# Optimization experiments

Hardware: AMD Instinct MI355X
Metric: run time of the kernel (lower is better)

Reference implementation:

```python
import jax, jax.numpy as jnp
import numpy as np

N = 100000
E = 1600000
IN_DIM, HID, OUT, HEADS, EDGE_DIM = 64, 32, 32, 4, 1


def setup_inputs() -> dict:
    key = jax.random.key(0)
    ks = jax.random.split(key, 24)
    p = lambda k, shape: (jax.random.normal(k, shape, dtype=jnp.float32) * 0.1)
    inp = {
        "x": jax.random.normal(ks[0], (N, IN_DIM), dtype=jnp.float32),
        "edge_index": jax.random.randint(ks[1], (2, E), 0, N, dtype=jnp.int32),
        "edge_attr": jax.random.uniform(ks[2], (E, EDGE_DIM), dtype=jnp.float32),
        # BatchNorm1d(edge_dim), eval mode
        "bn_gamma": jnp.ones((EDGE_DIM,), jnp.float32),
        "bn_beta": jnp.zeros((EDGE_DIM,), jnp.float32),
        "bn_mean": jnp.zeros((EDGE_DIM,), jnp.float32),
        "bn_var": jnp.ones((EDGE_DIM,), jnp.float32),
        # GATConv layer 1: in_dim -> hidden, heads=4, concat
        "W1": p(ks[3], (IN_DIM, HEADS * HID)),
        "as1": p(ks[4], (HEADS, HID)),
        "ad1": p(ks[5], (HEADS, HID)),
        "We1": p(ks[6], (EDGE_DIM, HEADS * HID)),
        "ae1": p(ks[7], (HEADS, HID)),
        "b1": jnp.zeros((HEADS * HID,), jnp.float32),
        # GATConv layer 2: heads*hidden -> out, heads=1, no concat
        "W2": p(ks[8], (HEADS * HID, OUT)),
        "as2": p(ks[9], (1, OUT)),
        "ad2": p(ks[10], (1, OUT)),
        "We2": p(ks[11], (EDGE_DIM, OUT)),
        "ae2": p(ks[12], (1, OUT)),
        "b2": jnp.zeros((OUT,), jnp.float32),
        # feature decoder MLP
        "Wd1": p(ks[13], (OUT, HID)),
        "bd1": jnp.zeros((HID,), jnp.float32),
        "Wd2": p(ks[14], (HID, IN_DIM)),
        "bd2": jnp.zeros((IN_DIM,), jnp.float32),
    }
    return inp


def gat_layer(x, src, dst, e, W, a_src, a_dst, We, a_e, b, heads, out_ch, concat):
    n = x.shape[0]
    h = (x @ W).reshape(n, heads, out_ch)                     # [N,H,C]
    alpha_src = (h * a_src).sum(-1)                           # [N,H]
    alpha_dst = (h * a_dst).sum(-1)                           # [N,H]
    he = (e @ We).reshape(-1, heads, out_ch)                  # [E,H,C]
    alpha = alpha_src[src] + alpha_dst[dst] + (he * a_e).sum(-1)  # [E,H]
    alpha = jax.nn.leaky_relu(alpha, 0.2)
    # segment softmax over destination node
    amax = jax.ops.segment_max(alpha, dst, num_segments=n)
    amax = jnp.where(jnp.isfinite(amax), amax, 0.0)
    ex = jnp.exp(alpha - amax[dst])
    denom = jax.ops.segment_sum(ex, dst, num_segments=n)
    att = ex / (denom[dst] + 1e-16)                           # [E,H]
    msg = h[src] * att[:, :, None]                            # [E,H,C]
    out = jax.ops.segment_sum(msg, dst, num_segments=n)       # [N,H,C]
    out = out.reshape(n, heads * out_ch) if concat else out.mean(axis=1)
    return out + b


def reference(x, edge_index, edge_attr, bn_gamma, bn_beta, bn_mean, bn_var,
              W1, as1, ad1, We1, ae1, b1, W2, as2, ad2, We2, ae2, b2,
              Wd1, bd1, Wd2, bd2):
    src, dst = edge_index[0], edge_index[1]
    # edge_norm(log1p(edge_attr)) with BatchNorm1d in eval mode
    e = (jnp.log1p(edge_attr) - bn_mean) * jax.lax.rsqrt(bn_var + 1e-5) * bn_gamma + bn_beta
    # encoder (dropout inactive in eval)
    h = gat_layer(x, src, dst, e, W1, as1, ad1, We1, ae1, b1, HEADS, HID, True)
    h = jax.nn.elu(h)
    z = gat_layer(h, src, dst, e, W2, as2, ad2, We2, ae2, b2, 1, OUT, False)
    # feature decoder MLP
    x_hat = jax.nn.elu(z @ Wd1 + bd1) @ Wd2 + bd2
    return (z, x_hat)
```

## Files before the change

kernel.cpp:

```cpp
#include <hip/hip_runtime.h>
#include <hip/hip_fp16.h>
#include <math.h>

#define NN 100000
#define NE 1600000

__global__ void k_hist(const int* __restrict__ ei, int* __restrict__ counts,
                       int* __restrict__ rank) {
    int e = blockIdx.x * blockDim.x + threadIdx.x;
    if (e < NE) rank[e] = atomicAdd(&counts[ei[NE + e]], 1);
}

__global__ void k_s1(const int* __restrict__ counts, int* __restrict__ bsum) {
    __shared__ int sd[256];
    int tid = threadIdx.x, b = blockIdx.x;
    int base = b * 2048 + tid * 8;
    int s = 0;
    #pragma unroll
    for (int j = 0; j < 8; ++j) {
        int g = base + j;
        s += (g < NN) ? counts[g] : 0;
    }
    sd[tid] = s;
    __syncthreads();
    for (int d = 128; d; d >>= 1) {
        if (tid < d) sd[tid] += sd[tid + d];
        __syncthreads();
    }
    if (tid == 0) bsum[b] = sd[0];
}

__global__ void k_s2(const int* __restrict__ bsum, int* __restrict__ boff,
                     int* __restrict__ rowptr,
                     const float* __restrict__ We1, const float* __restrict__ ae1,
                     const float* __restrict__ We2, const float* __restrict__ ae2,
                     float* __restrict__ wdot) {
    int t = threadIdx.x;
    if (t == 0) {
        int run = 0;
        for (int b = 0; b < 49; ++b) { boff[b] = run; run += bsum[b]; }
        rowptr[NN] = NE;
    }
    if (t >= 64 && t < 68) {
        int h = t - 64;
        float s = 0.f;
        for (int c = 0; c < 32; ++c) s += We1[h*32+c] * ae1[h*32+c];
        wdot[h] = s;
    } else if (t == 68) {
        float s = 0.f;
        for (int c = 0; c < 32; ++c) s += We2[c] * ae2[c];
        wdot[4] = s;
    }
}

__global__ void k_s3(const int* __restrict__ counts, const int* __restrict__ boff,
                     int* __restrict__ rowptr) {
    __shared__ int sT[256];
    int tid = threadIdx.x, b = blockIdx.x;
    int base = b * 2048 + tid * 8;
    int c[8];
    int s = 0;
    #pragma unroll
    for (int j = 0; j < 8; ++j) {
        int g = base + j;
        c[j] = (g < NN) ? counts[g] : 0;
        s += c[j];
    }
    sT[tid] = s;
    __syncthreads();
    for (int d = 1; d < 256; d <<= 1) {
        int v = (tid >= d) ? sT[tid - d] : 0;
        __syncthreads();
        sT[tid] += v;
        __syncthreads();
    }
    int run = (tid ? sT[tid - 1] : 0) + boff[b];
    #pragma unroll
    for (int j = 0; j < 8; ++j) {
        int g = base + j;
        if (g < NN) rowptr[g] = run;
        run += c[j];
    }
}

__global__ void k_scatter(const int* __restrict__ ei, const float* __restrict__ ea,
                          const float* __restrict__ g, const float* __restrict__ b,
                          const float* __restrict__ m, const float* __restrict__ v,
                          const int* __restrict__ rowptr, const int* __restrict__ rank,
                          int2* __restrict__ edges) {
    int e = blockIdx.x * blockDim.x + threadIdx.x;
    if (e >= NE) return;
    int dst = ei[NE + e];
    int pos = rowptr[dst] + rank[e];
    float en = (log1pf(ea[e]) - m[0]) * rsqrtf(v[0] + 1e-5f) * g[0] + b[0];
    edges[pos] = make_int2(ei[e], __float_as_int(en));
}

__global__ void __launch_bounds__(256, 2)
k1_node1(const float* __restrict__ x, const float* __restrict__ W1,
         const float* __restrict__ as1, const float* __restrict__ ad1,
         __half2* __restrict__ h1h, float* __restrict__ as1n,
         float* __restrict__ ad1n) {
    int tid = threadIdx.x, wid = tid >> 6, lane = tid & 63;
    float wc0[64], wc1[64];
    #pragma unroll
    for (int k = 0; k < 64; ++k) {
        wc0[k] = W1[k*128 + 2*lane];
        wc1[k] = W1[k*128 + 2*lane + 1];
    }
    float asc0 = as1[2*lane], asc1 = as1[2*lane+1];
    float adc0 = ad1[2*lane], adc1 = ad1[2*lane+1];
    int gw = (blockIdx.x << 2) + wid;
    int nw = gridDim.x << 2;
    for (int n = gw; n < NN; n += nw) {
        int nu = __builtin_amdgcn_readfirstlane(n);
        const float* xr = x + (size_t)nu * 64;
        float a0 = 0.f, a1 = 0.f;
        #pragma unroll
        for (int k = 0; k < 64; ++k) {
            float xk = xr[k];
            a0 = fmaf(xk, wc0[k], a0);
            a1 = fmaf(xk, wc1[k], a1);
        }
        h1h[(size_t)nu*64 + lane] = __float22half2_rn(make_float2(a0, a1));
        float p = a0*asc0 + a1*asc1;
        float q = a0*adc0 + a1*adc1;
        #pragma unroll
        for (int d = 1; d < 16; d <<= 1) {
            p += __shfl_xor(p, d);
            q += __shfl_xor(q, d);
        }
        if ((lane & 15) == 0) {
            int h = lane >> 4;
            as1n[nu*4 + h] = p;
            ad1n[nu*4 + h] = q;
        }
    }
}

__global__ void __launch_bounds__(256)
kA1(const int* __restrict__ rowptr, const int2* __restrict__ edges,
    const float* __restrict__ as1n, const float* __restrict__ ad1n,
    const float* __restrict__ wdot, const __half2* __restrict__ h1h,
    const float* __restrict__ b1, const float* __restrict__ W2,
    const float* __restrict__ as2, const float* __restrict__ ad2,
    __half2* __restrict__ h2h, float* __restrict__ as2n, float* __restrict__ ad2n) {
    __shared__ __half2 W2h[64*32];
    __shared__ float4 exs4[4][64];
    __shared__ int    srcl[4][64];
    __shared__ float  slot[4][128];
    int tid = threadIdx.x, wid = tid >> 6, lane = tid & 63;
    for (int i = tid; i < 2048; i += 256) {
        int k2 = i >> 5, c = i & 31;
        W2h[i] = __floats2half2_rn(W2[(2*k2)*32 + c], W2[(2*k2+1)*32 + c]);
    }
    __syncthreads();

    int n = blockIdx.x * 4 + wid;
    int row0 = rowptr[n], row1 = rowptr[n + 1];
    float4 wd  = *(const float4*)wdot;
    float4 adv = *(const float4*)&ad1n[n*4];
    int es = lane >> 5;
    int cq = lane & 31;
    int hq = cq >> 3;
    float den0 = 0.f, den1 = 0.f, den2 = 0.f, den3 = 0.f;
    float4 acc = make_float4(0.f, 0.f, 0.f, 0.f);
    const float* exf = (const float*)&exs4[wid][0];
    const uint2* h1u = (const uint2*)h1h;

    for (int base = row0; base < row1; base += 64) {
        int j = base + lane;
        bool val = j < row1;
        int2 ep = val ? edges[j] : make_int2(0, 0);
        int sv = ep.x;
        float ev = __int_as_float(ep.y);
        float4 asv = *(const float4*)&as1n[sv*4];
        float a0 = asv.x + adv.x + ev*wd.x; a0 = fmaxf(a0, 0.2f*a0);
        float a1 = asv.y + adv.y + ev*wd.y; a1 = fmaxf(a1, 0.2f*a1);
        float a2 = asv.z + adv.z + ev*wd.z; a2 = fmaxf(a2, 0.2f*a2);
        float a3 = asv.w + adv.w + ev*wd.w; a3 = fmaxf(a3, 0.2f*a3);
        float p0 = val ? __expf(a0) : 0.f; den0 += p0;
        float p1 = val ? __expf(a1) : 0.f; den1 += p1;
        float p2 = val ? __expf(a2) : 0.f; den2 += p2;
        float p3 = val ? __expf(a3) : 0.f; den3 += p3;
        exs4[wid][lane] = make_float4(p0, p1, p2, p3);
        srcl[wid][lane] = sv;

        int cnt = min(64, row1 - base);
        for (int i = 0; i < cnt; i += 2) {
            int idx = i + es;
            bool ok = idx < cnt;
            int s = srcl[wid][ok ? idx : i];
            float ex = ok ? exf[idx*4 + hq] : 0.f;
            uint2 u = h1u[(size_t)s*32 + cq];
            float2 hv01 = __half22float2(*(const __half2*)&u.x);
            float2 hv23 = __half22float2(*(const __half2*)&u.y);
            acc.x = fmaf(ex, hv01.x, acc.x);
            acc.y = fmaf(ex, hv01.y, acc.y);
            acc.z = fmaf(ex, hv23.x, acc.z);
            acc.w = fmaf(ex, hv23.y, acc.w);
        }
    }
    acc.x += __shfl_xor(acc.x, 32); acc.y += __shfl_xor(acc.y, 32);
    acc.z += __shfl_xor(acc.z, 32); acc.w += __shfl_xor(acc.w, 32);
    #pragma unroll
    for (int d = 32; d; d >>= 1) {
        den0 += __shfl_xor(den0, d); den1 += __shfl_xor(den1, d);
        den2 += __shfl_xor(den2, d); den3 += __shfl_xor(den3, d);
    }
    float dh = (hq == 0) ? den0 : (hq == 1) ? den1 : (hq == 2) ? den2 : den3;
    float r = 1.f / (dh + 1e-16f);
    float4 b1v = ((const float4*)b1)[cq];
    float o0 = acc.x * r + b1v.x; o0 = o0 > 0.f ? o0 : expm1f(o0);
    float o1 = acc.y * r + b1v.y; o1 = o1 > 0.f ? o1 : expm1f(o1);
    float o2 = acc.z * r + b1v.z; o2 = o2 > 0.f ? o2 : expm1f(o2);
    float o3 = acc.w * r + b1v.w; o3 = o3 > 0.f ? o3 : expm1f(o3);
    if (es == 0) *(float4*)&slot[wid][4*cq] = make_float4(o0, o1, o2, o3);

    int k2base = es * 32;
    float s2 = 0.f;
    #pragma unroll
    for (int kk = 0; kk < 32; ++kk) {
        float2 wf = __half22float2(W2h[(k2base + kk)*32 + cq]);
        s2 = fmaf(slot[wid][2*(k2base + kk)],     wf.x, s2);
        s2 = fmaf(slot[wid][2*(k2base + kk) + 1], wf.y, s2);
    }
    s2 += __shfl_xor(s2, 32);
    int l4 = lane & 15;
    float za = __shfl(s2, 2*l4);
    float zb = __shfl(s2, 2*l4 + 1);
    if (lane < 16) h2h[(size_t)n*16 + l4] = __float22half2_rn(make_float2(za, zb));
    float av = s2 * as2[cq] * 0.5f;
    float dv = s2 * ad2[cq] * 0.5f;
    #pragma unroll
    for (int d = 32; d; d >>= 1) { av += __shfl_xor(av, d); dv += __shfl_xor(dv, d); }
    if (lane == 0) { as2n[n] = av; ad2n[n] = dv; }
}

__global__ void __launch_bounds__(256)
kA2(const int* __restrict__ rowptr, const int2* __restrict__ edges,
    const float* __restrict__ as2n, const float* __restrict__ ad2n,
    const float* __restrict__ wdot, const __half2* __restrict__ h2h,
    const float* __restrict__ b2, const float* __restrict__ Wd1,
    const float* __restrict__ bd1, const float* __restrict__ Wd2,
    const float* __restrict__ bd2, float* __restrict__ out) {
    __shared__ float Wd1s[32*32], Wd2s[32*64];
    __shared__ float pl[4][64];
    __shared__ int   srcl[4][64];
    __shared__ float zs[4][32], ts[4][32];
    int tid = threadIdx.x, wid = tid >> 6, lane = tid & 63;
    int g = lane >> 4, l4 = lane & 15;
    int half = lane >> 5, l5 = lane & 31;
    for (int i = tid; i < 1024; i += 256) Wd1s[i] = Wd1[i];
    for (int i = tid; i < 2048; i += 256) Wd2s[i] = Wd2[i];
    __syncthreads();

    int n = blockIdx.x * 4 + wid;
    int row0 = rowptr[n], row1 = rowptr[n + 1];
    float wd4 = wdot[4];
    float adn = ad2n[n];
    float den = 0.f, acc0 = 0.f, acc1 = 0.f;

    for (int base = row0; base < row1; base += 64) {
        int j = base + lane;
        bool val = j < row1;
        int2 ep = val ? edges[j] : make_int2(0, 0);
        int sv = ep.x;
        float ev = __int_as_float(ep.y);
        float a = as2n[sv] + adn + ev * wd4;
        a = fmaxf(a, 0.2f*a);
        float p = val ? __expf(a) : 0.f;
        den += p;
        pl[wid][lane] = p;
        srcl[wid][lane] = sv;

        int cnt = min(64, row1 - base);
        for (int i = 0; i < cnt; i += 4) {
            int idx = i + g;
            bool ok = idx < cnt;
            int se   = ok ? srcl[wid][idx] : 0;
            float ex = ok ? pl[wid][idx] : 0.f;
            __half2 hv = h2h[(size_t)se*16 + l4];
            float2 hf = __half22float2(hv);
            acc0 = fmaf(ex, hf.x, acc0);
            acc1 = fmaf(ex, hf.y, acc1);
        }
    }
    #pragma unroll
    for (int d = 32; d; d >>= 1) den += __shfl_xor(den, d);
    acc0 += __shfl_xor(acc0, 16); acc0 += __shfl_xor(acc0, 32);
    acc1 += __shfl_xor(acc1, 16); acc1 += __shfl_xor(acc1, 32);
    float r = 1.f / (den + 1e-16f);
    if (lane < 16) {
        float z0 = acc0 * r + b2[2*l4];
        float z1 = acc1 * r + b2[2*l4 + 1];
        *(float2*)&out[(size_t)n*32 + 2*l4] = make_float2(z0, z1);
        *(float2*)&zs[wid][2*l4] = make_float2(z0, z1);
    }
    int kk0 = half * 16;
    float t2 = 0.f;
    #pragma unroll
    for (int k = 0; k < 16; ++k)
        t2 = fmaf(zs[wid][kk0 + k], Wd1s[(kk0 + k)*32 + l5], t2);
    t2 += __shfl_xor(t2, 32);
    t2 += bd1[l5];
    t2 = t2 > 0.f ? t2 : expm1f(t2);
    if (lane < 32) ts[wid][l5] = t2;

    float xo = bd2[lane];
    #pragma unroll
    for (int k = 0; k < 32; ++k)
        xo = fmaf(ts[wid][k], Wd2s[k*64 + lane], xo);
    out[(size_t)NN*32 + (size_t)n*64 + lane] = xo;
}

extern "C" void kernel_launch(void* const* d_in, const int* in_sizes, int n_in,
                              void* d_out, int out_size, void* d_ws, size_t ws_size,
                              hipStream_t stream) {
    const float* x    = (const float*)d_in[0];
    const int*   ei   = (const int*)  d_in[1];
    const float* ea   = (const float*)d_in[2];
    const float* bng  = (const float*)d_in[3];
    const float* bnb  = (const float*)d_in[4];
    const float* bnm  = (const float*)d_in[5];
    const float* bnv  = (const float*)d_in[6];
    const float* W1   = (const float*)d_in[7];
    const float* as1  = (const float*)d_in[8];
    const float* ad1  = (const float*)d_in[9];
    const float* We1  = (const float*)d_in[10];
    const float* ae1  = (const float*)d_in[11];
    const float* b1   = (const float*)d_in[12];
    const float* W2   = (const float*)d_in[13];
    const float* as2  = (const float*)d_in[14];
    const float* ad2  = (const float*)d_in[15];
    const float* We2  = (const float*)d_in[16];
    const float* ae2  = (const float*)d_in[17];
    const float* b2   = (const float*)d_in[18];
    const float* Wd1  = (const float*)d_in[19];
    const float* bd1  = (const float*)d_in[20];
    const float* Wd2  = (const float*)d_in[21];
    const float* bd2  = (const float*)d_in[22];
    float* out = (float*)d_out;

    float* wsf   = (float*)d_ws;
    __half2* h1h = (__half2*)wsf;
    float* as1n  = (float*)(h1h + (size_t)NN*64);
    float* ad1n  = as1n + (size_t)NN*4;
    __half2* h2h = (__half2*)(ad1n + (size_t)NN*4);
    float* as2n  = (float*)(h2h + (size_t)NN*16);
    float* ad2n  = as2n + NN;
    float* wdot  = ad2n + NN;
    int2*  edges = (int2*)(wdot + 8);
    int*   rank  = (int*)(edges + NE);
    int*   counts = rank + NE;
    int*   rowptr = counts + NN;
    int*   bsum   = rowptr + NN + 1;
    int*   boff   = bsum + 64;

    hipMemsetAsync(counts, 0, NN * sizeof(int), stream);
    hipLaunchKernelGGL(k_hist, dim3((NE+255)/256), dim3(256), 0, stream, ei, counts, rank);
    hipLaunchKernelGGL(k_s1, dim3(49), dim3(256), 0, stream, counts, bsum);
    hipLaunchKernelGGL(k_s2, dim3(1), dim3(128), 0, stream,
                       bsum, boff, rowptr, We1, ae1, We2, ae2, wdot);
    hipLaunchKernelGGL(k_s3, dim3(49), dim3(256), 0, stream, counts, boff, rowptr);
    hipLaunchKernelGGL(k_scatter, dim3((NE+255)/256), dim3(256), 0, stream,
                       ei, ea, bng, bnb, bnm, bnv, rowptr, rank, edges);
    hipLaunchKernelGGL(k1_node1, dim3(1024), dim3(256), 0, stream,
                       x, W1, as1, ad1, h1h, as1n, ad1n);
    hipLaunchKernelGGL(kA1, dim3(NN/4), dim3(256), 0, stream,
                       rowptr, edges, as1n, ad1n, wdot, h1h, b1, W2, as2, ad2,
                       h2h, as2n, ad2n);
    hipLaunchKernelGGL(kA2, dim3(NN/4), dim3(256), 0, stream,
                       rowptr, edges, as2n, ad2n, wdot, h2h, b2, Wd1, bd1, Wd2, bd2,
                       out);
}
```

Before: 395.2 us.

## Precompute edge attention exponentials in scatter and separate edge kernel

```diff
diff --git a/kernel.cpp b/kernel.cpp
--- a/kernel.cpp
+++ b/kernel.cpp
@@ -81,19 +81,6 @@
         if (g < NN) rowptr[g] = run;
         run += c[j];
     }
-}
-
-__global__ void k_scatter(const int* __restrict__ ei, const float* __restrict__ ea,
-                          const float* __restrict__ g, const float* __restrict__ b,
-                          const float* __restrict__ m, const float* __restrict__ v,
-                          const int* __restrict__ rowptr, const int* __restrict__ rank,
-                          int2* __restrict__ edges) {
-    int e = blockIdx.x * blockDim.x + threadIdx.x;
-    if (e >= NE) return;
-    int dst = ei[NE + e];
-    int pos = rowptr[dst] + rank[e];
-    float en = (log1pf(ea[e]) - m[0]) * rsqrtf(v[0] + 1e-5f) * g[0] + b[0];
-    edges[pos] = make_int2(ei[e], __float_as_int(en));
 }
 
 __global__ void __launch_bounds__(256, 2)
@@ -138,10 +125,40 @@
     }
 }
 
+__global__ void k_scatter(const int* __restrict__ ei, const float* __restrict__ ea,
+                          const float* __restrict__ g, const float* __restrict__ b,
+                          const float* __restrict__ m, const float* __restrict__ v,
+                          const int* __restrict__ rowptr, const int* __restrict__ rank,
+                          const float* __restrict__ as1n, const float* __restrict__ ad1n,
+                          const float* __restrict__ wdot,
+                          int* __restrict__ src_s, int* __restrict__ dst_s,
+                          float* __restrict__ en_s, uint2* __restrict__ exh4) {
+    int e = blockIdx.x * blockDim.x + threadIdx.x;
+    if (e >= NE) return;
+    int src = ei[e], dst = ei[NE + e];
+    int pos = rowptr[dst] + rank[e];
+    float en = (log1pf(ea[e]) - m[0]) * rsqrtf(v[0] + 1e-5f) * g[0] + b[0];
+    float4 wd  = *(const float4*)wdot;
+    float4 asv = *(const float4*)&as1n[src*4];
+    float4 adv = *(const float4*)&ad1n[dst*4];
+    float a0 = asv.x + adv.x + en*wd.x; a0 = fmaxf(a0, 0.2f*a0);
+    float a1 = asv.y + adv.y + en*wd.y; a1 = fmaxf(a1, 0.2f*a1);
+    float a2 = asv.z + adv.z + en*wd.z; a2 = fmaxf(a2, 0.2f*a2);
+    float a3 = asv.w + adv.w + en*wd.w; a3 = fmaxf(a3, 0.2f*a3);
+    __half2 p01 = __floats2half2_rn(__expf(a0), __expf(a1));
+    __half2 p23 = __floats2half2_rn(__expf(a2), __expf(a3));
+    uint2 pk;
+    pk.x = *(const unsigned int*)&p01;
+    pk.y = *(const unsigned int*)&p23;
+    src_s[pos] = src;
+    dst_s[pos] = dst;
+    en_s[pos]  = en;
+    exh4[pos]  = pk;
+}
+
 __global__ void __launch_bounds__(256)
-kA1(const int* __restrict__ rowptr, const int2* __restrict__ edges,
-    const float* __restrict__ as1n, const float* __restrict__ ad1n,
-    const float* __restrict__ wdot, const __half2* __restrict__ h1h,
+kA1(const int* __restrict__ rowptr, const int* __restrict__ src_s,
+    const uint2* __restrict__ exh4, const __half2* __restrict__ h1h,
     const float* __restrict__ b1, const float* __restrict__ W2,
     const float* __restrict__ as2, const float* __restrict__ ad2,
     __half2* __restrict__ h2h, float* __restrict__ as2n, float* __restrict__ ad2n) {
@@ -158,8 +175,6 @@
 
     int n = blockIdx.x * 4 + wid;
     int row0 = rowptr[n], row1 = rowptr[n + 1];
-    float4 wd  = *(const float4*)wdot;
-    float4 adv = *(const float4*)&ad1n[n*4];
     int es = lane >> 5;
     int cq = lane & 31;
     int hq = cq >> 3;
@@ -171,19 +186,12 @@
     for (int base = row0; base < row1; base += 64) {
         int j = base + lane;
         bool val = j < row1;
-        int2 ep = val ? edges[j] : make_int2(0, 0);
-        int sv = ep.x;
-        float ev = __int_as_float(ep.y);
-        float4 asv = *(const float4*)&as1n[sv*4];
-        float a0 = asv.x + adv.x + ev*wd.x; a0 = fmaxf(a0, 0.2f*a0);
-        float a1 = asv.y + adv.y + ev*wd.y; a1 = fmaxf(a1, 0.2f*a1);
-        float a2 = asv.z + adv.z + ev*wd.z; a2 = fmaxf(a2, 0.2f*a2);
-        float a3 = asv.w + adv.w + ev*wd.w; a3 = fmaxf(a3, 0.2f*a3);
-        float p0 = val ? __expf(a0) : 0.f; den0 += p0;
-        float p1 = val ? __expf(a1) : 0.f; den1 += p1;
-        float p2 = val ? __expf(a2) : 0.f; den2 += p2;
-        float p3 = val ? __expf(a3) : 0.f; den3 += p3;
-        exs4[wid][lane] = make_float4(p0, p1, p2, p3);
+        int sv = val ? src_s[j] : 0;
+        uint2 eu = val ? exh4[j] : make_uint2(0u, 0u);
+        float2 e01 = __half22float2(*(const __half2*)&eu.x);
+        float2 e23 = __half22float2(*(const __half2*)&eu.y);
+        den0 += e01.x; den1 += e01.y; den2 += e23.x; den3 += e23.y;
+        exs4[wid][lane] = make_float4(e01.x, e01.y, e23.x, e23.y);
         srcl[wid][lane] = sv;
 
         int cnt = min(64, row1 - base);
@@ -237,10 +245,20 @@
     if (lane == 0) { as2n[n] = av; ad2n[n] = dv; }
 }
 
+__global__ void kE2(const int* __restrict__ src_s, const int* __restrict__ dst_s,
+                    const float* __restrict__ en_s, const float* __restrict__ as2n,
+                    const float* __restrict__ ad2n, const float* __restrict__ wdot,
+                    __half* __restrict__ exh2) {
+    int e = blockIdx.x * blockDim.x + threadIdx.x;
+    if (e >= NE) return;
+    float a = as2n[src_s[e]] + ad2n[dst_s[e]] + en_s[e] * wdot[4];
+    a = fmaxf(a, 0.2f*a);
+    exh2[e] = __float2half(__expf(a));
+}
+
 __global__ void __launch_bounds__(256)
-kA2(const int* __restrict__ rowptr, const int2* __restrict__ edges,
-    const float* __restrict__ as2n, const float* __restrict__ ad2n,
-    const float* __restrict__ wdot, const __half2* __restrict__ h2h,
+kA2(const int* __restrict__ rowptr, const int* __restrict__ src_s,
+    const __half* __restrict__ exh2, const __half2* __restrict__ h2h,
     const float* __restrict__ b2, const float* __restrict__ Wd1,
     const float* __restrict__ bd1, const float* __restrict__ Wd2,
     const float* __restrict__ bd2, float* __restrict__ out) {
@@ -257,19 +275,13 @@
 
     int n = blockIdx.x * 4 + wid;
     int row0 = rowptr[n], row1 = rowptr[n + 1];
-    float wd4 = wdot[4];
-    float adn = ad2n[n];
     float den = 0.f, acc0 = 0.f, acc1 = 0.f;
 
     for (int base = row0; base < row1; base += 64) {
         int j = base + lane;
         bool val = j < row1;
-        int2 ep = val ? edges[j] : make_int2(0, 0);
-        int sv = ep.x;
-        float ev = __int_as_float(ep.y);
-        float a = as2n[sv] + adn + ev * wd4;
-        a = fmaxf(a, 0.2f*a);
-        float p = val ? __expf(a) : 0.f;
+        int sv  = val ? src_s[j] : 0;
+        float p = val ? __half2float(exh2[j]) : 0.f;
         den += p;
         pl[wid][lane] = p;
         srcl[wid][lane] = sv;
@@ -342,20 +354,24 @@
     const float* bd2  = (const float*)d_in[22];
     float* out = (float*)d_out;
 
-    float* wsf   = (float*)d_ws;
-    __half2* h1h = (__half2*)wsf;
-    float* as1n  = (float*)(h1h + (size_t)NN*64);
-    float* ad1n  = as1n + (size_t)NN*4;
-    __half2* h2h = (__half2*)(ad1n + (size_t)NN*4);
-    float* as2n  = (float*)(h2h + (size_t)NN*16);
-    float* ad2n  = as2n + NN;
-    float* wdot  = ad2n + NN;
-    int2*  edges = (int2*)(wdot + 8);
-    int*   rank  = (int*)(edges + NE);
-    int*   counts = rank + NE;
-    int*   rowptr = counts + NN;
-    int*   bsum   = rowptr + NN + 1;
-    int*   boff   = bsum + 64;
+    char* wsb = (char*)d_ws;
+    __half2* h1h = (__half2*)wsb;
+    float* as1n  = (float*)(wsb += (size_t)NN*64*4);
+    float* ad1n  = (float*)(wsb += (size_t)NN*4*4);
+    __half2* h2h = (__half2*)(wsb += (size_t)NN*4*4);
+    float* as2n  = (float*)(wsb += (size_t)NN*16*4);
+    float* ad2n  = (float*)(wsb += (size_t)NN*4);
+    float* wdot  = (float*)(wsb += (size_t)NN*4);
+    uint2* exh4  = (uint2*)(wsb += 8*4);
+    int* src_s   = (int*)(wsb += (size_t)NE*8);
+    int* dst_s   = (int*)(wsb += (size_t)NE*4);
+    float* en_s  = (float*)(wsb += (size_t)NE*4);
+    __half* exh2 = (__half*)(wsb += (size_t)NE*4);
+    int* rank    = (int*)(wsb += (size_t)NE*2);
+    int* counts  = (int*)(wsb += (size_t)NE*4);
+    int* rowptr  = (int*)(wsb += (size_t)NN*4);
+    int* bsum    = (int*)(wsb += (size_t)(NN+1)*4);
+    int* boff    = (int*)(wsb += 64*4);
 
     hipMemsetAsync(counts, 0, NN * sizeof(int), stream);
     hipLaunchKernelGGL(k_hist, dim3((NE+255)/256), dim3(256), 0, stream, ei, counts, rank);
@@ -363,14 +379,17 @@
     hipLaunchKernelGGL(k_s2, dim3(1), dim3(128), 0, stream,
                        bsum, boff, rowptr, We1, ae1, We2, ae2, wdot);
     hipLaunchKernelGGL(k_s3, dim3(49), dim3(256), 0, stream, counts, boff, rowptr);
-    hipLaunchKernelGGL(k_scatter, dim3((NE+255)/256), dim3(256), 0, stream,
-                       ei, ea, bng, bnb, bnm, bnv, rowptr, rank, edges);
     hipLaunchKernelGGL(k1_node1, dim3(1024), dim3(256), 0, stream,
                        x, W1, as1, ad1, h1h, as1n, ad1n);
+    hipLaunchKernelGGL(k_scatter, dim3((NE+255)/256), dim3(256), 0, stream,
+                       ei, ea, bng, bnb, bnm, bnv, rowptr, rank,
+                       as1n, ad1n, wdot, src_s, dst_s, en_s, exh4);
     hipLaunchKernelGGL(kA1, dim3(NN/4), dim3(256), 0, stream,
-                       rowptr, edges, as1n, ad1n, wdot, h1h, b1, W2, as2, ad2,
+                       rowptr, src_s, exh4, h1h, b1, W2, as2, ad2,
                        h2h, as2n, ad2n);
+    hipLaunchKernelGGL(kE2, dim3((NE+255)/256), dim3(256), 0, stream,
+                       src_s, dst_s, en_s, as2n, ad2n, wdot, exh2);
     hipLaunchKernelGGL(kA2, dim3(NN/4), dim3(256), 0, stream,
-                       rowptr, edges, as2n, ad2n, wdot, h2h, b2, Wd1, bd1, Wd2, bd2,
+                       rowptr, src_s, exh2, h2h, b2, Wd1, bd1, Wd2, bd2,
                        out);
 }
```

After: 485.7 us. 22.9% more time.
